# Performance work log

Hardware: AMD Instinct MI355X
Metric: run time of the kernel (lower is better)

## Reference

```python
import jax, jax.numpy as jnp
import numpy as np

B, T, H, NUM_TAGS = 16, 2048, 1024, 74
RATE_HEAD, RATE_MID = 0.88, 0.7


def _make_segments(rng):
    """Build ragged word segmentation as dense index/mask tensors.

    word_idx[b, t]  : index j of the word covering char position t
    is_head[b, t]   : True iff t is the first char of its word segment
    valid_mask[b, t]: True iff t < length of utterance b
    """
    word_idx = np.zeros((B, T), dtype=np.int32)
    is_head = np.zeros((B, T), dtype=bool)
    valid = np.zeros((B, T), dtype=bool)
    for b in range(B):
        length = int(rng.integers(T // 2, T + 1))
        s, j = 0, 0
        while s < length:
            seg = int(rng.integers(1, 5))  # jieba-like segments of 1..4 chars
            seg = min(seg, length - s)
            word_idx[b, s:s + seg] = j
            is_head[b, s] = True
            valid[b, s:s + seg] = True
            s += seg
            j += 1
    return word_idx, is_head, valid


def setup_inputs() -> dict:
    key = jax.random.key(0)
    k1, k2, k3 = jax.random.split(key, 3)
    rng = np.random.default_rng(0)
    word_idx, is_head, valid = _make_segments(rng)
    return {
        "out_char": jax.random.normal(k1, (B, T, H), dtype=jnp.float32),
        "out_word": jax.random.normal(k2, (B, T, H), dtype=jnp.float32),
        "word_idx": jnp.asarray(word_idx),
        "is_head": jnp.asarray(is_head),
        "valid_mask": jnp.asarray(valid),
        "W_out": jax.random.normal(k3, (H, NUM_TAGS), dtype=jnp.float32) / np.sqrt(H),
        "b_out": jnp.zeros((NUM_TAGS,), dtype=jnp.float32),
    }


def reference(out_char, out_word, word_idx, is_head, valid_mask, W_out, b_out):
    # Feat_Merge: fused gather-scale-scatter over ragged word segments.
    # rate = rate_head on the first char of each segment, rate_mid elsewhere.
    rate = jnp.where(is_head, RATE_HEAD, RATE_MID).astype(out_char.dtype)  # [B, T]
    gathered = jnp.take_along_axis(out_word, word_idx[:, :, None], axis=1)  # [B, T, H]
    feat = gathered * rate[:, :, None] + out_char * (1.0 - rate)[:, :, None]
    feat = jnp.where(valid_mask[:, :, None], feat, 0.0)  # zeros beyond length (as in feat_B init)
    # Output tagging projection (dropout p=0 at inference)
    logits = jnp.einsum("bth,hk->btk", feat, W_out) + b_out  # [B, T, num_tags]
    return logits
```

## Files before the change

### kernel.cpp

```cpp
#include <hip/hip_runtime.h>
#include <hip/hip_bf16.h>

#define TT 2048
#define HH 1024
#define NTAGS 74
#define NPAD 80
#define CHK 64
#define NCH (HH / CHK)
#define MROWS 64
#define THREADS 256
#define NXCD 8

typedef __bf16 bf16x8 __attribute__((ext_vector_type(8)));
typedef float f32x4 __attribute__((ext_vector_type(4)));

__global__ __launch_bounds__(256) void prep_w_kernel(const float* __restrict__ W,
                                                     __bf16* __restrict__ Wt) {
    __shared__ float tile[64][80];
    const int k0 = blockIdx.x * 64;
    const int tid = threadIdx.x;
    for (int i = tid; i < 64 * NTAGS; i += 256) {
        int k = i / NTAGS, n = i - k * NTAGS;
        tile[k][n] = W[(k0 + k) * NTAGS + n];
    }
    __syncthreads();
    for (int i = tid; i < NPAD * 64; i += 256) {
        int n = i >> 6, kk = i & 63;
        float v = (n < NTAGS) ? tile[kk][n] : 0.0f;
        Wt[n * HH + k0 + kk] = (__bf16)v;
    }
}

__global__ __launch_bounds__(256, 2) void slu_main(const float* __restrict__ out_char,
                                                   const float* __restrict__ out_word,
                                                   const int* __restrict__ word_idx,
                                                   const int* __restrict__ is_head,
                                                   const int* __restrict__ valid_mask,
                                                   const __bf16* __restrict__ Wt,
                                                   const float* __restrict__ b_out,
                                                   float* __restrict__ out) {
    __shared__ __align__(16) char smem[45056];
    const int tid = threadIdx.x;
    const int wv = tid >> 6;
    const int lane = tid & 63;
    const int l15 = lane & 15;
    const int kgrp = lane >> 4;

    const int bid = blockIdx.x;
    const int rb = (bid & (NXCD - 1)) * (512 / NXCD) + (bid >> 3);
    const int rowbase = rb * MROWS;

    const int rloc = tid >> 2;
    const int q = tid & 3;
    const int r = rowbase + rloc;
    const int bq = r >> 11;
    const int widx = word_idx[r];
    const int val = valid_mask[r];

    if (!__syncthreads_or(val)) {
        for (int i = tid; i < MROWS * NTAGS; i += THREADS) {
            const int rr = i / NTAGS, cc = i - rr * NTAGS;
            out[(size_t)(rowbase + rr) * NTAGS + cc] = b_out[cc];
        }
        return;
    }

    const float rt = is_head[r] ? 0.88f : 0.70f;
    const float rate = val ? rt : 0.0f;
    const float crate = val ? (1.0f - rt) : 0.0f;
    const float* cptr = out_char + (size_t)r * HH + q * 16;
    const float* wptr = out_word + ((size_t)bq * TT + widx) * HH + q * 16;
    const int asw = (rloc & 7) << 4;
    const int awr0 = (rloc * 128 + q * 32) ^ asw;
    const int awr1 = (rloc * 128 + q * 32 + 16) ^ asw;

    const int wn0 = tid >> 3, wsb = tid & 7;
    const __bf16* wgp0 = Wt + (size_t)wn0 * HH + wsb * 8;
    const __bf16* wgp1 = wgp0 + 32 * HH;
    const __bf16* wgp2 = wgp0 + 64 * HH;
    const int wsw = (wn0 & 7) << 4;
    const int wwr0 = (wn0 * 128 + wsb * 16) ^ wsw;
    const int wwr1 = ((wn0 + 32) * 128 + wsb * 16) ^ wsw;
    const int wwr2 = ((wn0 + 64) * 128 + wsb * 16) ^ wsw;
    const bool w3 = (tid < 128);

    const int fsw = (l15 & 7) << 4;
    const int arow = wv * 16 + l15;
    int aoff[2], woff[2][5];
#pragma unroll
    for (int s = 0; s < 2; ++s) {
        aoff[s] = (arow * 128 + s * 64 + kgrp * 16) ^ fsw;
#pragma unroll
        for (int nt = 0; nt < 5; ++nt)
            woff[s][nt] = ((nt * 16 + l15) * 128 + s * 64 + kgrp * 16) ^ fsw;
    }

    f32x4 acc[5];
#pragma unroll
    for (int nt = 0; nt < 5; ++nt) acc[nt] = (f32x4){0.f, 0.f, 0.f, 0.f};

    float4 ac[4], aw[4];
    bf16x8 wreg0, wreg1, wreg2;

    {
        float4 c0[4], w0[4];
        if (val) {
#pragma unroll
            for (int i = 0; i < 4; ++i) {
                c0[i] = *(const float4*)(cptr + i * 4);
                w0[i] = *(const float4*)(wptr + i * 4);
            }
        }
        bf16x8 wr0 = *(const bf16x8*)(wgp0);
        bf16x8 wr1 = *(const bf16x8*)(wgp1);
        bf16x8 wr2 = w3 ? *(const bf16x8*)(wgp2) : (bf16x8)0;
        bf16x8 f0, f1;
        if (val) {
#pragma unroll
            for (int i = 0; i < 2; ++i) {
                f0[i * 4 + 0] = (__bf16)(w0[i].x * rate + c0[i].x * crate);
                f0[i * 4 + 1] = (__bf16)(w0[i].y * rate + c0[i].y * crate);
                f0[i * 4 + 2] = (__bf16)(w0[i].z * rate + c0[i].z * crate);
                f0[i * 4 + 3] = (__bf16)(w0[i].w * rate + c0[i].w * crate);
                f1[i * 4 + 0] = (__bf16)(w0[i + 2].x * rate + c0[i + 2].x * crate);
                f1[i * 4 + 1] = (__bf16)(w0[i + 2].y * rate + c0[i + 2].y * crate);
                f1[i * 4 + 2] = (__bf16)(w0[i + 2].z * rate + c0[i + 2].z * crate);
                f1[i * 4 + 3] = (__bf16)(w0[i + 2].w * rate + c0[i + 2].w * crate);
            }
        } else {
            f0 = (bf16x8)0; f1 = (bf16x8)0;
        }
        *(bf16x8*)(smem + awr0) = f0;
        *(bf16x8*)(smem + awr1) = f1;
        *(bf16x8*)(smem + 24576 + wwr0) = wr0;
        *(bf16x8*)(smem + 24576 + wwr1) = wr1;
        if (w3) *(bf16x8*)(smem + 24576 + wwr2) = wr2;
        if (val) {
#pragma unroll
            for (int i = 0; i < 4; ++i) {
                ac[i] = *(const float4*)(cptr + CHK + i * 4);
                aw[i] = *(const float4*)(wptr + CHK + i * 4);
            }
        }
        wreg0 = *(const bf16x8*)(wgp0 + CHK);
        wreg1 = *(const bf16x8*)(wgp1 + CHK);
        wreg2 = w3 ? *(const bf16x8*)(wgp2 + CHK) : (bf16x8)0;
    }
    __syncthreads();

    for (int ch = 0; ch < NCH; ++ch) {
        if (ch + 1 < NCH) {
            char* An = smem + ((ch + 1) % 3) * 8192;
            char* Wn = smem + 24576 + ((ch + 1) & 1) * 10240;
            bf16x8 f0, f1;
            if (val) {
#pragma unroll
                for (int i = 0; i < 2; ++i) {
                    f0[i * 4 + 0] = (__bf16)(aw[i].x * rate + ac[i].x * crate);
                    f0[i * 4 + 1] = (__bf16)(aw[i].y * rate + ac[i].y * crate);
                    f0[i * 4 + 2] = (__bf16)(aw[i].z * rate + ac[i].z * crate);
                    f0[i * 4 + 3] = (__bf16)(aw[i].w * rate + ac[i].w * crate);
                    f1[i * 4 + 0] = (__bf16)(aw[i + 2].x * rate + ac[i + 2].x * crate);
                    f1[i * 4 + 1] = (__bf16)(aw[i + 2].y * rate + ac[i + 2].y * crate);
                    f1[i * 4 + 2] = (__bf16)(aw[i + 2].z * rate + ac[i + 2].z * crate);
                    f1[i * 4 + 3] = (__bf16)(aw[i + 2].w * rate + ac[i + 2].w * crate);
                }
            } else {
                f0 = (bf16x8)0; f1 = (bf16x8)0;
            }
            *(bf16x8*)(An + awr0) = f0;
            *(bf16x8*)(An + awr1) = f1;
            *(bf16x8*)(Wn + wwr0) = wreg0;
            *(bf16x8*)(Wn + wwr1) = wreg1;
            if (w3) *(bf16x8*)(Wn + wwr2) = wreg2;
        }
        if (ch + 2 < NCH) {
            const int ko = (ch + 2) * CHK;
            if (val) {
#pragma unroll
                for (int i = 0; i < 4; ++i) {
                    ac[i] = *(const float4*)(cptr + ko + i * 4);
                    aw[i] = *(const float4*)(wptr + ko + i * 4);
                }
            }
            wreg0 = *(const bf16x8*)(wgp0 + ko);
            wreg1 = *(const bf16x8*)(wgp1 + ko);
            wreg2 = w3 ? *(const bf16x8*)(wgp2 + ko) : (bf16x8)0;
        }
        const char* Ab = smem + (ch % 3) * 8192;
        const char* Wb = smem + 24576 + (ch & 1) * 10240;
#pragma unroll
        for (int s = 0; s < 2; ++s) {
            bf16x8 a = *(const bf16x8*)(Ab + aoff[s]);
#pragma unroll
            for (int nt = 0; nt < 5; ++nt) {
                bf16x8 bw = *(const bf16x8*)(Wb + woff[s][nt]);
                acc[nt] = __builtin_amdgcn_mfma_f32_16x16x32_bf16(a, bw, acc[nt], 0, 0, 0);
            }
        }
        __syncthreads();
    }

    const int orow = rowbase + wv * 16 + kgrp * 4;
#pragma unroll
    for (int nt = 0; nt < 5; ++nt) {
        const int col = nt * 16 + l15;
        if (col < NTAGS) {
            const float bias = b_out[col];
#pragma unroll
            for (int i = 0; i < 4; ++i) {
                out[(size_t)(orow + i) * NTAGS + col] = acc[nt][i] + bias;
            }
        }
    }
}

extern "C" void kernel_launch(void* const* d_in, const int* in_sizes, int n_in,
                              void* d_out, int out_size, void* d_ws, size_t ws_size,
                              hipStream_t stream) {
    const float* out_char = (const float*)d_in[0];
    const float* out_word = (const float*)d_in[1];
    const int* word_idx = (const int*)d_in[2];
    const int* is_head = (const int*)d_in[3];
    const int* valid_mask = (const int*)d_in[4];
    const float* W_out = (const float*)d_in[5];
    const float* b_out = (const float*)d_in[6];
    float* out = (float*)d_out;
    __bf16* Wt = (__bf16*)d_ws;

    prep_w_kernel<<<HH / 64, 256, 0, stream>>>(W_out, Wt);

    const int rows = 16 * TT;
    slu_main<<<rows / MROWS, THREADS, 0, stream>>>(out_char, out_word, word_idx, is_head,
                                                   valid_mask, Wt, b_out, out);
}
```

Baseline: 35.30 us.

## Stage unique word rows once per tile and blend from LDS

Instead of gathering one out_word row per character, each 64-row tile loads only the contiguous range of distinct word rows it covers into LDS, computed from a wave-wide max of word_idx. The rate blend moves into the MFMA operand path, using the LDS copies of out_char and out_word. This aims to cut global traffic for out_word, since words span 1-4 chars. The cost is more LDS, extra per-element blend arithmetic before each MFMA, and double rounding through bf16 before the blend.

```diff
diff --git a/kernel.cpp b/kernel.cpp
--- a/kernel.cpp
+++ b/kernel.cpp
@@ -39,7 +39,7 @@
                                                    const __bf16* __restrict__ Wt,
                                                    const float* __restrict__ b_out,
                                                    float* __restrict__ out) {
-    __shared__ __align__(16) char smem[45056];
+    __shared__ __align__(16) char smem[53248];
     const int tid = threadIdx.x;
     const int wv = tid >> 6;
     const int lane = tid & 63;
@@ -49,12 +49,12 @@
     const int bid = blockIdx.x;
     const int rb = (bid & (NXCD - 1)) * (512 / NXCD) + (bid >> 3);
     const int rowbase = rb * MROWS;
+    const int batch = rowbase >> 11;
+    const size_t batbase = (size_t)batch * TT;
 
     const int rloc = tid >> 2;
     const int q = tid & 3;
     const int r = rowbase + rloc;
-    const int bq = r >> 11;
-    const int widx = word_idx[r];
     const int val = valid_mask[r];
 
     if (!__syncthreads_or(val)) {
@@ -65,14 +65,22 @@
         return;
     }
 
-    const float rt = is_head[r] ? 0.88f : 0.70f;
-    const float rate = val ? rt : 0.0f;
-    const float crate = val ? (1.0f - rt) : 0.0f;
+    int wmaxv = word_idx[rowbase + lane];
+#pragma unroll
+    for (int m = 1; m < 64; m <<= 1) {
+        const int o = __shfl_xor(wmaxv, m);
+        wmaxv = (o > wmaxv) ? o : wmaxv;
+    }
+    const int w0 = word_idx[rowbase];
+    const int nw = wmaxv - w0 + 1;
+
     const float* cptr = out_char + (size_t)r * HH + q * 16;
-    const float* wptr = out_word + ((size_t)bq * TT + widx) * HH + q * 16;
-    const int asw = (rloc & 7) << 4;
-    const int awr0 = (rloc * 128 + q * 32) ^ asw;
-    const int awr1 = (rloc * 128 + q * 32 + 16) ^ asw;
+    const int csw = (rloc & 7) << 4;
+    const int cwr0 = (rloc * 128 + q * 32) ^ csw;
+    const int cwr1 = (rloc * 128 + q * 32 + 16) ^ csw;
+
+    const bool wstage = (rloc < nw);
+    const float* uptr = out_word + (batbase + w0 + rloc) * HH + q * 16;
 
     const int wn0 = tid >> 3, wsb = tid & 7;
     const __bf16* wgp0 = Wt + (size_t)wn0 * HH + wsb * 8;
@@ -84,63 +92,79 @@
     const int wwr2 = ((wn0 + 64) * 128 + wsb * 16) ^ wsw;
     const bool w3 = (tid < 128);
 
-    const int fsw = (l15 & 7) << 4;
-    const int arow = wv * 16 + l15;
-    int aoff[2], woff[2][5];
+    const int myrow = rowbase + wv * 16 + l15;
+    const int myval = valid_mask[myrow];
+    const float rt = is_head[myrow] ? 0.88f : 0.70f;
+    const float rate = myval ? rt : 0.0f;
+    const float crate = myval ? (1.0f - rt) : 0.0f;
+    int u_my = word_idx[myrow] - w0;
+    if (u_my < 0) u_my = 0;
+
+    const int mysw = (l15 & 7) << 4;
+    const int usw2 = (u_my & 7) << 4;
+    int cfo[2], ufo[2], woff[2][5];
 #pragma unroll
     for (int s = 0; s < 2; ++s) {
-        aoff[s] = (arow * 128 + s * 64 + kgrp * 16) ^ fsw;
+        cfo[s] = ((wv * 16 + l15) * 128 + s * 64 + kgrp * 16) ^ mysw;
+        ufo[s] = (u_my * 128 + s * 64 + kgrp * 16) ^ usw2;
 #pragma unroll
         for (int nt = 0; nt < 5; ++nt)
-            woff[s][nt] = ((nt * 16 + l15) * 128 + s * 64 + kgrp * 16) ^ fsw;
+            woff[s][nt] = ((nt * 16 + l15) * 128 + s * 64 + kgrp * 16) ^ mysw;
     }
 
     f32x4 acc[5];
 #pragma unroll
     for (int nt = 0; nt < 5; ++nt) acc[nt] = (f32x4){0.f, 0.f, 0.f, 0.f};
 
-    float4 ac[4], aw[4];
+    float4 cc[4], uc[4];
     bf16x8 wreg0, wreg1, wreg2;
 
+#define PACK2(dst0, dst1, src, pred)                                     \
+    {                                                                    \
+        bf16x8 f0_, f1_;                                                 \
+        if (pred) {                                                      \
+            _Pragma("unroll") for (int i_ = 0; i_ < 2; ++i_) {           \
+                f0_[i_ * 4 + 0] = (__bf16)src[i_].x;                     \
+                f0_[i_ * 4 + 1] = (__bf16)src[i_].y;                     \
+                f0_[i_ * 4 + 2] = (__bf16)src[i_].z;                     \
+                f0_[i_ * 4 + 3] = (__bf16)src[i_].w;                     \
+                f1_[i_ * 4 + 0] = (__bf16)src[i_ + 2].x;                 \
+                f1_[i_ * 4 + 1] = (__bf16)src[i_ + 2].y;                 \
+                f1_[i_ * 4 + 2] = (__bf16)src[i_ + 2].z;                 \
+                f1_[i_ * 4 + 3] = (__bf16)src[i_ + 2].w;                 \
+            }                                                            \
+        } else {                                                         \
+            f0_ = (bf16x8)0; f1_ = (bf16x8)0;                            \
+        }                                                                \
+        *(bf16x8*)(dst0) = f0_;                                          \
+        *(bf16x8*)(dst1) = f1_;                                          \
+    }
+
     {
-        float4 c0[4], w0[4];
+        float4 c0[4], u0[4];
         if (val) {
 #pragma unroll
-            for (int i = 0; i < 4; ++i) {
-                c0[i] = *(const float4*)(cptr + i * 4);
-                w0[i] = *(const float4*)(wptr + i * 4);
-            }
+            for (int i = 0; i < 4; ++i) c0[i] = *(const float4*)(cptr + i * 4);
+        }
+        if (wstage) {
+#pragma unroll
+            for (int i = 0; i < 4; ++i) u0[i] = *(const float4*)(uptr + i * 4);
         }
         bf16x8 wr0 = *(const bf16x8*)(wgp0);
         bf16x8 wr1 = *(const bf16x8*)(wgp1);
         bf16x8 wr2 = w3 ? *(const bf16x8*)(wgp2) : (bf16x8)0;
-        bf16x8 f0, f1;
+        PACK2(smem + cwr0, smem + cwr1, c0, val);
+        if (wstage) PACK2(smem + 16384 + cwr0, smem + 16384 + cwr1, u0, true);
+        *(bf16x8*)(smem + 32768 + wwr0) = wr0;
+        *(bf16x8*)(smem + 32768 + wwr1) = wr1;
+        if (w3) *(bf16x8*)(smem + 32768 + wwr2) = wr2;
         if (val) {
 #pragma unroll
-            for (int i = 0; i < 2; ++i) {
-                f0[i * 4 + 0] = (__bf16)(w0[i].x * rate + c0[i].x * crate);
-                f0[i * 4 + 1] = (__bf16)(w0[i].y * rate + c0[i].y * crate);
-                f0[i * 4 + 2] = (__bf16)(w0[i].z * rate + c0[i].z * crate);
-                f0[i * 4 + 3] = (__bf16)(w0[i].w * rate + c0[i].w * crate);
-                f1[i * 4 + 0] = (__bf16)(w0[i + 2].x * rate + c0[i + 2].x * crate);
-                f1[i * 4 + 1] = (__bf16)(w0[i + 2].y * rate + c0[i + 2].y * crate);
-                f1[i * 4 + 2] = (__bf16)(w0[i + 2].z * rate + c0[i + 2].z * crate);
-                f1[i * 4 + 3] = (__bf16)(w0[i + 2].w * rate + c0[i + 2].w * crate);
-            }
-        } else {
-            f0 = (bf16x8)0; f1 = (bf16x8)0;
-        }
-        *(bf16x8*)(smem + awr0) = f0;
-        *(bf16x8*)(smem + awr1) = f1;
-        *(bf16x8*)(smem + 24576 + wwr0) = wr0;
-        *(bf16x8*)(smem + 24576 + wwr1) = wr1;
-        if (w3) *(bf16x8*)(smem + 24576 + wwr2) = wr2;
-        if (val) {
-#pragma unroll
-            for (int i = 0; i < 4; ++i) {
-                ac[i] = *(const float4*)(cptr + CHK + i * 4);
-                aw[i] = *(const float4*)(wptr + CHK + i * 4);
-            }
+            for (int i = 0; i < 4; ++i) cc[i] = *(const float4*)(cptr + CHK + i * 4);
+        }
+        if (wstage) {
+#pragma unroll
+            for (int i = 0; i < 4; ++i) uc[i] = *(const float4*)(uptr + CHK + i * 4);
         }
         wreg0 = *(const bf16x8*)(wgp0 + CHK);
         wreg1 = *(const bf16x8*)(wgp1 + CHK);
@@ -150,26 +174,11 @@
 
     for (int ch = 0; ch < NCH; ++ch) {
         if (ch + 1 < NCH) {
-            char* An = smem + ((ch + 1) % 3) * 8192;
-            char* Wn = smem + 24576 + ((ch + 1) & 1) * 10240;
-            bf16x8 f0, f1;
-            if (val) {
-#pragma unroll
-                for (int i = 0; i < 2; ++i) {
-                    f0[i * 4 + 0] = (__bf16)(aw[i].x * rate + ac[i].x * crate);
-                    f0[i * 4 + 1] = (__bf16)(aw[i].y * rate + ac[i].y * crate);
-                    f0[i * 4 + 2] = (__bf16)(aw[i].z * rate + ac[i].z * crate);
-                    f0[i * 4 + 3] = (__bf16)(aw[i].w * rate + ac[i].w * crate);
-                    f1[i * 4 + 0] = (__bf16)(aw[i + 2].x * rate + ac[i + 2].x * crate);
-                    f1[i * 4 + 1] = (__bf16)(aw[i + 2].y * rate + ac[i + 2].y * crate);
-                    f1[i * 4 + 2] = (__bf16)(aw[i + 2].z * rate + ac[i + 2].z * crate);
-                    f1[i * 4 + 3] = (__bf16)(aw[i + 2].w * rate + ac[i + 2].w * crate);
-                }
-            } else {
-                f0 = (bf16x8)0; f1 = (bf16x8)0;
-            }
-            *(bf16x8*)(An + awr0) = f0;
-            *(bf16x8*)(An + awr1) = f1;
+            char* Cn = smem + ((ch + 1) & 1) * 8192;
+            char* Un = smem + 16384 + ((ch + 1) & 1) * 8192;
+            char* Wn = smem + 32768 + ((ch + 1) & 1) * 10240;
+            PACK2(Cn + cwr0, Cn + cwr1, cc, val);
+            if (wstage) PACK2(Un + cwr0, Un + cwr1, uc, true);
             *(bf16x8*)(Wn + wwr0) = wreg0;
             *(bf16x8*)(Wn + wwr1) = wreg1;
             if (w3) *(bf16x8*)(Wn + wwr2) = wreg2;
@@ -178,20 +187,27 @@
             const int ko = (ch + 2) * CHK;
             if (val) {
 #pragma unroll
-                for (int i = 0; i < 4; ++i) {
-                    ac[i] = *(const float4*)(cptr + ko + i * 4);
-                    aw[i] = *(const float4*)(wptr + ko + i * 4);
-                }
+                for (int i = 0; i < 4; ++i) cc[i] = *(const float4*)(cptr + ko + i * 4);
+            }
+            if (wstage) {
+#pragma unroll
+                for (int i = 0; i < 4; ++i) uc[i] = *(const float4*)(uptr + ko + i * 4);
             }
             wreg0 = *(const bf16x8*)(wgp0 + ko);
             wreg1 = *(const bf16x8*)(wgp1 + ko);
             wreg2 = w3 ? *(const bf16x8*)(wgp2 + ko) : (bf16x8)0;
         }
-        const char* Ab = smem + (ch % 3) * 8192;
-        const char* Wb = smem + 24576 + (ch & 1) * 10240;
+        const char* Cb = smem + (ch & 1) * 8192;
+        const char* Ub = smem + 16384 + (ch & 1) * 8192;
+        const char* Wb = smem + 32768 + (ch & 1) * 10240;
 #pragma unroll
         for (int s = 0; s < 2; ++s) {
-            bf16x8 a = *(const bf16x8*)(Ab + aoff[s]);
+            bf16x8 cf = *(const bf16x8*)(Cb + cfo[s]);
+            bf16x8 uf = *(const bf16x8*)(Ub + ufo[s]);
+            bf16x8 a;
+#pragma unroll
+            for (int e = 0; e < 8; ++e)
+                a[e] = (__bf16)((float)uf[e] * rate + (float)cf[e] * crate);
 #pragma unroll
             for (int nt = 0; nt < 5; ++nt) {
                 bf16x8 bw = *(const bf16x8*)(Wb + woff[s][nt]);
@@ -213,6 +229,7 @@
             }
         }
     }
+#undef PACK2
 }
 
 extern "C" void kernel_launch(void* const* d_in, const int* in_sizes, int n_in,
```

Measured after the change: 35.86 us. Within noise of the previous version (+1.6%).
